# Kernel optimization log

Measured on AMD Instinct MI355X. Metric: run time of the kernel, lower is better.

## Reference

```python
import jax, jax.numpy as jnp
import numpy as np

D_MODEL = 1024
NHEAD = 16
HEAD_DIM = D_MODEL // NHEAD
NEG = -1e9
LN_EPS = 1e-5


def setup_inputs() -> dict:
    key = jax.random.key(0)
    ks = jax.random.split(key, 12)
    B, S, D = 2, 2048, D_MODEL
    scale = 1.0 / np.sqrt(D)
    inp = {
        "x": jax.random.normal(ks[0], (B, S, D), jnp.float32),
        "mask": jax.random.randint(ks[1], (B, S), 0, 2, jnp.int32),
        "wq": jax.random.normal(ks[2], (D, D), jnp.float32) * scale,
        "bq": jnp.zeros((D,), jnp.float32),
        "wk": jax.random.normal(ks[3], (D, D), jnp.float32) * scale,
        "bk": jnp.zeros((D,), jnp.float32),
        "wv": jax.random.normal(ks[4], (D, D), jnp.float32) * scale,
        "bv": jnp.zeros((D,), jnp.float32),
        "wo": jax.random.normal(ks[5], (D, D), jnp.float32) * scale,
        "bo": jnp.zeros((D,), jnp.float32),
        "attn_bias": jax.random.normal(ks[6], (1, NHEAD, 1, 1), jnp.float32) * 0.02,
        "ln_g": jnp.ones((D,), jnp.float32),
        "ln_b": jnp.zeros((D,), jnp.float32),
    }
    return inp


def _layer_norm(x, g, b):
    mu = jnp.mean(x, axis=-1, keepdims=True)
    var = jnp.var(x, axis=-1, keepdims=True)
    return (x - mu) * jax.lax.rsqrt(var + LN_EPS) * g + b


def reference(x, mask, wq, bq, wk, bk, wv, bv, wo, bo, attn_bias, ln_g, ln_b):
    B, S, D = x.shape
    H, Hd = NHEAD, HEAD_DIM
    # QKV projections -> [B, H, S, Hd]
    q = (x @ wq + bq).reshape(B, S, H, Hd).transpose(0, 2, 1, 3)
    k = (x @ wk + bk).reshape(B, S, H, Hd).transpose(0, 2, 1, 3)
    v = (x @ wv + bv).reshape(B, S, H, Hd).transpose(0, 2, 1, 3)
    # Scores [B, H, S, S] with per-head scalar bias
    scores = jnp.einsum("bhsd,bhtd->bhst", q, k) / jnp.sqrt(jnp.float32(Hd))
    scores = scores + attn_bias
    # mask [B,S] -> [B,1,1,S]; masked_fill where mask == 0
    m = (mask[:, None, None, :] == 0)
    scores = jnp.where(m, jnp.float32(NEG), scores)
    attn = jax.nn.softmax(scores, axis=-1)  # dropout = identity (eval)
    out = jnp.einsum("bhst,bhtd->bhsd", attn, v)
    out = out.transpose(0, 2, 1, 3).reshape(B, S, D)
    out = out @ wo + bo
    return _layer_norm(x + out, ln_g, ln_b)
```

## Files before the change

### kernel.cpp

```cpp
#include <hip/hip_runtime.h>

typedef __attribute__((ext_vector_type(8))) short short8;
typedef __attribute__((ext_vector_type(4))) float f32x4;
typedef __attribute__((ext_vector_type(16))) float f32x16;
typedef __attribute__((ext_vector_type(4))) unsigned short us4;

#define DEV __device__ __forceinline__

#define GLD16(gp, lp) __builtin_amdgcn_global_load_lds( \
    (const __attribute__((address_space(1))) void*)(gp), \
    (__attribute__((address_space(3))) void*)(lp), 16, 0, 0)

DEV unsigned short f2bf(float f) {
    union { float f; unsigned u; } v; v.f = f;
    unsigned r = v.u + 0x7fffu + ((v.u >> 16) & 1u);
    return (unsigned short)(r >> 16);
}

DEV float bf2f(unsigned short u) {
    union { unsigned u; float f; } v; v.u = (unsigned)u << 16;
    return v.f;
}

DEV float fexp2(float x) {
#if __has_builtin(__builtin_amdgcn_exp2f)
    return __builtin_amdgcn_exp2f(x);
#else
    return __expf(x * 0.69314718056f);
#endif
}

__global__ __launch_bounds__(256) void k_convert(const float* __restrict__ x,
                                                 unsigned short* __restrict__ xb) {
    int i = blockIdx.x * 256 + threadIdx.x;
    float4 v = ((const float4*)x)[i];
    us4 o = { f2bf(v.x), f2bf(v.y), f2bf(v.z), f2bf(v.w) };
    ((us4*)xb)[i] = o;
}

__global__ __launch_bounds__(256) void k_transw(const float* __restrict__ wq, const float* __restrict__ wk,
                                                const float* __restrict__ wv, const float* __restrict__ wo,
                                                unsigned short* __restrict__ wt) {
    __shared__ float tile[32][33];
    const int z = blockIdx.z;
    const float* src = (z == 0) ? wq : (z == 1) ? wk : (z == 2) ? wv : wo;
    unsigned short* dst = wt + (size_t)z * (1u << 20);
    const int n0 = blockIdx.x * 32, k0 = blockIdx.y * 32;
    const int tx = threadIdx.x, ty = threadIdx.y;
#pragma unroll
    for (int i = 0; i < 4; ++i)
        tile[ty + i * 8][tx] = src[(size_t)(k0 + ty + i * 8) * 1024 + n0 + tx];
    __syncthreads();
#pragma unroll
    for (int i = 0; i < 4; ++i)
        dst[(size_t)(n0 + ty + i * 8) * 1024 + k0 + tx] = f2bf(tile[tx][ty + i * 8]);
}

__global__ __launch_bounds__(256) void k_gemm_qkv(const unsigned short* __restrict__ A,
                                                  const unsigned short* __restrict__ Wt,
                                                  const float* __restrict__ bq,
                                                  const float* __restrict__ bk,
                                                  const float* __restrict__ bv,
                                                  unsigned short* __restrict__ Qo,
                                                  unsigned short* __restrict__ Ko,
                                                  unsigned short* __restrict__ Vo,
                                                  float qscale) {
    __shared__ unsigned short lA[2][128 * 32];
    __shared__ unsigned short lB[2][3][64 * 32];
    const int m0 = blockIdx.y * 128, n0 = blockIdx.x * 64;
    const int tid = threadIdx.x;
    const int lane = tid & 63;
    const int w = tid >> 6, wm = w >> 1, wn = w & 1;

    const int arow0 = tid >> 2, acl = tid & 3;
    const int arow1 = (tid + 256) >> 2;
    const int brow = tid >> 2;
    const unsigned short* agp0 = A + (size_t)(m0 + arow0) * 1024 + acl * 8;
    const unsigned short* agp1 = A + (size_t)(m0 + arow1) * 1024 + acl * 8;
    const unsigned short* bgp[3];
#pragma unroll
    for (int z = 0; z < 3; ++z)
        bgp[z] = Wt + ((size_t)z << 20) + (size_t)(n0 + brow) * 1024 + acl * 8;
    const int apc0 = ((arow0 << 2) | (acl ^ ((arow0 >> 1) & 3))) * 8;
    const int apc1 = ((arow1 << 2) | (acl ^ ((arow1 >> 1) & 3))) * 8;
    const int bpc  = ((brow  << 2) | (acl ^ ((brow  >> 1) & 3))) * 8;

    int ach[4], bch[2];
#pragma unroll
    for (int mt = 0; mt < 4; ++mt) {
        int row = wm * 64 + mt * 16 + (lane & 15);
        ach[mt] = ((row << 2) | ((lane >> 4) ^ ((row >> 1) & 3))) * 8;
    }
#pragma unroll
    for (int nt = 0; nt < 2; ++nt) {
        int row = wn * 32 + nt * 16 + (lane & 15);
        bch[nt] = ((row << 2) | ((lane >> 4) ^ ((row >> 1) & 3))) * 8;
    }

    f32x4 acc[3][4][2] = {};
    short8 ra0 = *(const short8*)agp0;
    short8 ra1 = *(const short8*)agp1;
    short8 rb[3];
#pragma unroll
    for (int z = 0; z < 3; ++z) rb[z] = *(const short8*)bgp[z];

    for (int t = 0; t < 32; ++t) {
        unsigned short* sA = lA[t & 1];
        *(short8*)(sA + apc0) = ra0;
        *(short8*)(sA + apc1) = ra1;
#pragma unroll
        for (int z = 0; z < 3; ++z)
            *(short8*)(lB[t & 1][z] + bpc) = rb[z];
        if (t < 31) {
            ra0 = *(const short8*)(agp0 + (t + 1) * 32);
            ra1 = *(const short8*)(agp1 + (t + 1) * 32);
#pragma unroll
            for (int z = 0; z < 3; ++z) rb[z] = *(const short8*)(bgp[z] + (t + 1) * 32);
        }
        __syncthreads();
        short8 af[4], bf[3][2];
#pragma unroll
        for (int mt = 0; mt < 4; ++mt) af[mt] = *(const short8*)(sA + ach[mt]);
#pragma unroll
        for (int z = 0; z < 3; ++z)
#pragma unroll
            for (int nt = 0; nt < 2; ++nt) bf[z][nt] = *(const short8*)(lB[t & 1][z] + bch[nt]);
#pragma unroll
        for (int z = 0; z < 3; ++z)
#pragma unroll
            for (int mt = 0; mt < 4; ++mt)
#pragma unroll
                for (int nt = 0; nt < 2; ++nt)
                    acc[z][mt][nt] = __builtin_amdgcn_mfma_f32_16x16x32_bf16(af[mt], bf[z][nt], acc[z][mt][nt], 0, 0, 0);
    }

#pragma unroll
    for (int z = 0; z < 3; ++z) {
        const float* bias = (z == 0) ? bq : (z == 1) ? bk : bv;
        const float scl = (z == 0) ? qscale : 1.0f;
        unsigned short* outp = (z == 0) ? Qo : (z == 1) ? Ko : Vo;
#pragma unroll
        for (int nt = 0; nt < 2; ++nt) {
            const int col = n0 + wn * 32 + nt * 16 + (lane & 15);
            const float bvv = bias[col];
            const int h = col >> 6, hd = col & 63;
#pragma unroll
            for (int mt = 0; mt < 4; ++mt) {
#pragma unroll
                for (int r = 0; r < 4; ++r) {
                    const int row = m0 + wm * 64 + mt * 16 + (lane >> 4) * 4 + r;
                    const int b = row >> 11, s = row & 2047;
                    const float v = (acc[z][mt][nt][r] + bvv) * scl;
                    if (z == 2)
                        outp[(size_t)((b * 16 + h) * 64 + hd) * 2048 + s] = f2bf(v);
                    else
                        outp[(size_t)((b * 16 + h) * 2048 + s) * 64 + hd] = f2bf(v);
                }
            }
        }
    }
}

__global__ __launch_bounds__(256) void k_gemm_o(const unsigned short* __restrict__ A,
                                                const unsigned short* __restrict__ Wt,
                                                const float* __restrict__ bias,
                                                unsigned short* __restrict__ out) {
    __shared__ unsigned short lA[2][128 * 32];
    __shared__ unsigned short lB[2][64 * 32];
    const int m0 = blockIdx.y * 128, n0 = blockIdx.x * 64;
    const int tid = threadIdx.x;
    const int lane = tid & 63;
    const int w = tid >> 6, wm = w >> 1, wn = w & 1;

    const int arow0 = tid >> 2, acl = tid & 3;
    const int arow1 = (tid + 256) >> 2;
    const int brow = tid >> 2;
    const unsigned short* agp0 = A + (size_t)(m0 + arow0) * 1024 + acl * 8;
    const unsigned short* agp1 = A + (size_t)(m0 + arow1) * 1024 + acl * 8;
    const unsigned short* bgp  = Wt + (size_t)(n0 + brow) * 1024 + acl * 8;
    const int apc0 = ((arow0 << 2) | (acl ^ ((arow0 >> 1) & 3))) * 8;
    const int apc1 = ((arow1 << 2) | (acl ^ ((arow1 >> 1) & 3))) * 8;
    const int bpc  = ((brow  << 2) | (acl ^ ((brow  >> 1) & 3))) * 8;

    int ach[4], bch[2];
#pragma unroll
    for (int mt = 0; mt < 4; ++mt) {
        int row = wm * 64 + mt * 16 + (lane & 15);
        ach[mt] = ((row << 2) | ((lane >> 4) ^ ((row >> 1) & 3))) * 8;
    }
#pragma unroll
    for (int nt = 0; nt < 2; ++nt) {
        int row = wn * 32 + nt * 16 + (lane & 15);
        bch[nt] = ((row << 2) | ((lane >> 4) ^ ((row >> 1) & 3))) * 8;
    }

    f32x4 acc[4][2] = {};
    short8 ra0 = *(const short8*)agp0;
    short8 ra1 = *(const short8*)agp1;
    short8 rb0 = *(const short8*)bgp;

    for (int t = 0; t < 32; ++t) {
        unsigned short* sA = lA[t & 1];
        unsigned short* sB = lB[t & 1];
        *(short8*)(sA + apc0) = ra0;
        *(short8*)(sA + apc1) = ra1;
        *(short8*)(sB + bpc)  = rb0;
        if (t < 31) {
            ra0 = *(const short8*)(agp0 + (t + 1) * 32);
            ra1 = *(const short8*)(agp1 + (t + 1) * 32);
            rb0 = *(const short8*)(bgp  + (t + 1) * 32);
        }
        __syncthreads();
        short8 af[4], bf[2];
#pragma unroll
        for (int mt = 0; mt < 4; ++mt) af[mt] = *(const short8*)(sA + ach[mt]);
#pragma unroll
        for (int nt = 0; nt < 2; ++nt) bf[nt] = *(const short8*)(sB + bch[nt]);
#pragma unroll
        for (int mt = 0; mt < 4; ++mt)
#pragma unroll
            for (int nt = 0; nt < 2; ++nt)
                acc[mt][nt] = __builtin_amdgcn_mfma_f32_16x16x32_bf16(af[mt], bf[nt], acc[mt][nt], 0, 0, 0);
    }

#pragma unroll
    for (int nt = 0; nt < 2; ++nt) {
        const int col = n0 + wn * 32 + nt * 16 + (lane & 15);
        const float bv = bias[col];
#pragma unroll
        for (int mt = 0; mt < 4; ++mt)
#pragma unroll
            for (int r = 0; r < 4; ++r) {
                const int row = m0 + wm * 64 + mt * 16 + (lane >> 4) * 4 + r;
                out[(size_t)row * 1024 + col] = f2bf(acc[mt][nt][r] + bv);
            }
    }
}

__global__ __launch_bounds__(256, 4) void k_attn(const unsigned short* __restrict__ Qb,
                                                 const unsigned short* __restrict__ Kb,
                                                 const unsigned short* __restrict__ Vt,
                                                 const int* __restrict__ mask,
                                                 const float* __restrict__ attn_bias,
                                                 unsigned short* __restrict__ po0,
                                                 unsigned short* __restrict__ po1,
                                                 float* __restrict__ lp0,
                                                 float* __restrict__ lp1) {
    __shared__ unsigned short ksm[2 * 4096];
    __shared__ unsigned short vsm[2 * 4096];
    __shared__ float addb[1024];
    const int id = blockIdx.x;
    const int xcd = id & 7, slot = id >> 3;
    const int half = slot & 1, qt = (slot >> 1) & 15, bh = xcd * 4 + (slot >> 5);
    const int b = bh >> 4, h = bh & 15;
    const int tid = threadIdx.x, l = tid & 63, w = tid >> 6;
    const int q = l & 31, hi = l >> 5;

    {
        const float hb = attn_bias[h] * 1.44269504f;
        int4 m = ((const int4*)(mask + b * 2048 + half * 1024))[tid];
        float4 a = { m.x ? hb : -1e30f, m.y ? hb : -1e30f,
                     m.z ? hb : -1e30f, m.w ? hb : -1e30f };
        ((float4*)addb)[tid] = a;
    }

    const size_t bhS = (size_t)bh * 2048;
    const unsigned short* Kbh = Kb + (bhS + half * 1024) * 64;
    const unsigned short* Vbh = Vt + (size_t)bh * 64 * 2048;
    const int q0 = qt * 128 + w * 32;

    const int srow = l >> 3;
    const int sxor = 8 * ((l & 7) ^ ((l >> 3) & 7));
    const unsigned short* Ksrc = Kbh + (size_t)(w * 16 + srow) * 64 + sxor;
    const unsigned short* Vsrc = Vbh + (size_t)(w * 16 + srow) * 2048 + half * 1024 + sxor;
    unsigned short* lk0 = ksm + w * 1024;
    unsigned short* lv0 = vsm + w * 1024;

#define STAGE(kt_, buf_) { \
    const unsigned short* gk = Ksrc + (size_t)(kt_) * 4096; \
    const unsigned short* gv = Vsrc + (kt_) * 64; \
    unsigned short* lk = lk0 + (buf_) * 4096; \
    unsigned short* lv = lv0 + (buf_) * 4096; \
    GLD16(gk, lk); GLD16(gk + 512, lk + 512); \
    GLD16(gv, lv); GLD16(gv + 16384, lv + 512); }

    int kro[2][4], vro[2][2][2];
#pragma unroll
    for (int sub = 0; sub < 2; ++sub) {
#pragma unroll
        for (int db = 0; db < 4; ++db) {
            int key = q + sub * 32;
            kro[sub][db] = key * 128 + ((db * 32 + hi * 16) ^ ((key & 7) << 4));
        }
#pragma unroll
        for (int kg = 0; kg < 2; ++kg)
#pragma unroll
            for (int dh = 0; dh < 2; ++dh) {
                int row = q + dh * 32;
                vro[sub][kg][dh] = row * 128 + ((sub * 64 + kg * 32 + hi * 16) ^ ((row & 7) << 4));
            }
    }

    short8 qf[4];
#pragma unroll
    for (int db = 0; db < 4; ++db)
        qf[db] = *(const short8*)(Qb + (bhS + q0 + q) * 64 + db * 16 + hi * 8);

    f32x16 o0 = {}, o1 = {};
    float4 ls = { 0.f, 0.f, 0.f, 0.f };

    STAGE(0, 0);
    __syncthreads();

    for (int kt = 0; kt < 16; ++kt) {
        const int cur = kt & 1;
        if (kt < 15) STAGE(kt + 1, cur ^ 1);
        const char* kb = (const char*)(ksm + cur * 4096);
        const char* vb = (const char*)(vsm + cur * 4096);
        const float* abp = addb + kt * 64;
#pragma unroll
        for (int sub = 0; sub < 2; ++sub) {
            short8 kf0 = *(const short8*)(kb + kro[sub][0]);
            short8 kf1 = *(const short8*)(kb + kro[sub][1]);
            short8 kf2 = *(const short8*)(kb + kro[sub][2]);
            short8 kf3 = *(const short8*)(kb + kro[sub][3]);
            f32x16 sa0 = {}, sa1 = {};
            __builtin_amdgcn_s_setprio(1);
            sa0 = __builtin_amdgcn_mfma_f32_32x32x16_bf16(kf0, qf[0], sa0, 0, 0, 0);
            sa1 = __builtin_amdgcn_mfma_f32_32x32x16_bf16(kf1, qf[1], sa1, 0, 0, 0);
            sa0 = __builtin_amdgcn_mfma_f32_32x32x16_bf16(kf2, qf[2], sa0, 0, 0, 0);
            sa1 = __builtin_amdgcn_mfma_f32_32x32x16_bf16(kf3, qf[3], sa1, 0, 0, 0);
            __builtin_amdgcn_s_setprio(0);
            float p[16];
#pragma unroll
            for (int rr = 0; rr < 4; ++rr) {
                float4 ab = *(const float4*)(abp + sub * 32 + rr * 8 + hi * 4);
                p[rr * 4 + 0] = fexp2(sa0[rr * 4 + 0] + sa1[rr * 4 + 0] + ab.x);
                p[rr * 4 + 1] = fexp2(sa0[rr * 4 + 1] + sa1[rr * 4 + 1] + ab.y);
                p[rr * 4 + 2] = fexp2(sa0[rr * 4 + 2] + sa1[rr * 4 + 2] + ab.z);
                p[rr * 4 + 3] = fexp2(sa0[rr * 4 + 3] + sa1[rr * 4 + 3] + ab.w);
            }
#pragma unroll
            for (int r = 0; r < 16; r += 4) {
                ls.x += p[r]; ls.y += p[r + 1]; ls.z += p[r + 2]; ls.w += p[r + 3];
            }
#pragma unroll
            for (int kg = 0; kg < 2; ++kg) {
                unsigned P0, P1, P2, P3;
                asm("v_cvt_pk_bf16_f32 %0, %1, %2" : "=v"(P0) : "v"(p[kg * 8 + 0]), "v"(p[kg * 8 + 1]));
                asm("v_cvt_pk_bf16_f32 %0, %1, %2" : "=v"(P1) : "v"(p[kg * 8 + 2]), "v"(p[kg * 8 + 3]));
                asm("v_cvt_pk_bf16_f32 %0, %1, %2" : "=v"(P2) : "v"(p[kg * 8 + 4]), "v"(p[kg * 8 + 5]));
                asm("v_cvt_pk_bf16_f32 %0, %1, %2" : "=v"(P3) : "v"(p[kg * 8 + 6]), "v"(p[kg * 8 + 7]));
                asm("v_permlane32_swap_b32 %0, %1" : "+v"(P0), "+v"(P2));
                asm("v_permlane32_swap_b32 %0, %1" : "+v"(P1), "+v"(P3));
                union { unsigned u[4]; short8 s8; } af;
                af.u[0] = P0; af.u[1] = P1; af.u[2] = P2; af.u[3] = P3;
                short8 vf0 = *(const short8*)(vb + vro[sub][kg][0]);
                short8 vf1 = *(const short8*)(vb + vro[sub][kg][1]);
                __builtin_amdgcn_s_setprio(1);
                o0 = __builtin_amdgcn_mfma_f32_32x32x16_bf16(af.s8, vf0, o0, 0, 0, 0);
                o1 = __builtin_amdgcn_mfma_f32_32x32x16_bf16(af.s8, vf1, o1, 0, 0, 0);
                __builtin_amdgcn_s_setprio(0);
            }
        }
        __syncthreads();
    }
#undef STAGE

    float lsum = ls.x + ls.y + ls.z + ls.w;
    lsum += __shfl_xor(lsum, 32, 64);
    float* lpx = half ? lp1 : lp0;
    if (hi == 0) lpx[bhS + q0 + q] = lsum;
    unsigned short* pop = (half ? po1 : po0) + ((size_t)b * 2048 + q0) * 1024 + h * 64 + q;
#pragma unroll
    for (int r = 0; r < 16; ++r) {
        int qrow = (r & 3) + 8 * (r >> 2) + 4 * hi;
        pop[(size_t)qrow * 1024] = f2bf(o0[r]);
        pop[(size_t)qrow * 1024 + 32] = f2bf(o1[r]);
    }
}

__global__ __launch_bounds__(256) void k_comb(const unsigned short* __restrict__ po0,
                                              const unsigned short* __restrict__ po1,
                                              const float* __restrict__ lp0,
                                              const float* __restrict__ lp1,
                                              unsigned short* __restrict__ ao) {
    const int idx8 = blockIdx.x * 256 + threadIdx.x;
    const int e = idx8 * 8;
    const int row = e >> 10, c = e & 1023;
    const int h = c >> 6, b = row >> 11, s = row & 2047;
    const size_t li = ((size_t)(b * 16 + h) << 11) + s;
    const float rinv = __builtin_amdgcn_rcpf(lp0[li] + lp1[li]);
    short8 a0 = ((const short8*)po0)[idx8];
    short8 a1 = ((const short8*)po1)[idx8];
    short8 o;
#pragma unroll
    for (int j = 0; j < 8; ++j)
        o[j] = (short)f2bf((bf2f((unsigned short)a0[j]) + bf2f((unsigned short)a1[j])) * rinv);
    ((short8*)ao)[idx8] = o;
}

__global__ __launch_bounds__(256) void k_ln(const float* __restrict__ x, const unsigned short* __restrict__ op,
                                            const float* __restrict__ g, const float* __restrict__ be,
                                            float* __restrict__ out) {
    const int row = blockIdx.x, tid = threadIdx.x;
    const float4 xv = ((const float4*)(x + (size_t)row * 1024))[tid];
    const us4 ov = ((const us4*)(op + (size_t)row * 1024))[tid];
    float4 v = { xv.x + bf2f(ov.x), xv.y + bf2f(ov.y), xv.z + bf2f(ov.z), xv.w + bf2f(ov.w) };
    float sum = v.x + v.y + v.z + v.w;
    float ss = v.x * v.x + v.y * v.y + v.z * v.z + v.w * v.w;
#pragma unroll
    for (int xm = 1; xm < 64; xm <<= 1) {
        sum += __shfl_xor(sum, xm, 64);
        ss += __shfl_xor(ss, xm, 64);
    }
    __shared__ float red[8];
    const int lane = tid & 63, w = tid >> 6;
    if (lane == 0) { red[w] = sum; red[4 + w] = ss; }
    __syncthreads();
    sum = red[0] + red[1] + red[2] + red[3];
    ss = red[4] + red[5] + red[6] + red[7];
    const float mu = sum * (1.0f / 1024.0f);
    const float rstd = rsqrtf(ss * (1.0f / 1024.0f) - mu * mu + 1e-5f);
    const float4 gv = ((const float4*)g)[tid];
    const float4 bv = ((const float4*)be)[tid];
    float4 o = { (v.x - mu) * rstd * gv.x + bv.x, (v.y - mu) * rstd * gv.y + bv.y,
                 (v.z - mu) * rstd * gv.z + bv.z, (v.w - mu) * rstd * gv.w + bv.w };
    ((float4*)(out + (size_t)row * 1024))[tid] = o;
}

extern "C" void kernel_launch(void* const* d_in, const int* in_sizes, int n_in,
                              void* d_out, int out_size, void* d_ws, size_t ws_size,
                              hipStream_t stream) {
    const float* x        = (const float*)d_in[0];
    const int*   mask     = (const int*)d_in[1];
    const float* wq       = (const float*)d_in[2];
    const float* bq       = (const float*)d_in[3];
    const float* wk       = (const float*)d_in[4];
    const float* bk       = (const float*)d_in[5];
    const float* wv       = (const float*)d_in[6];
    const float* bv       = (const float*)d_in[7];
    const float* wo       = (const float*)d_in[8];
    const float* bo       = (const float*)d_in[9];
    const float* attnb    = (const float*)d_in[10];
    const float* ln_g     = (const float*)d_in[11];
    const float* ln_b     = (const float*)d_in[12];

    char* ws = (char*)d_ws;
    unsigned short* xb  = (unsigned short*)(ws);
    unsigned short* wt  = (unsigned short*)(ws + (8ll  << 20));
    unsigned short* qb  = (unsigned short*)(ws + (16ll << 20));
    unsigned short* kb  = (unsigned short*)(ws + (24ll << 20));
    unsigned short* vtb = (unsigned short*)(ws + (32ll << 20));
    unsigned short* po1 = (unsigned short*)(ws + (40ll << 20));
    float*          lp0 = (float*)(ws + (48ll << 20));
    float*          lp1 = (float*)(ws + (48ll << 20) + (256ll << 10));
    unsigned short* po0 = xb;
    unsigned short* ao  = qb;
    unsigned short* opj = kb;

    const float qscale = 0.125f * 1.44269504f;

    k_convert<<<4096, 256, 0, stream>>>(x, xb);
    k_transw<<<dim3(32, 32, 4), dim3(32, 8), 0, stream>>>(wq, wk, wv, wo, wt);
    k_gemm_qkv<<<dim3(16, 32), 256, 0, stream>>>(xb, wt, bq, bk, bv, qb, kb, vtb, qscale);
    k_attn<<<1024, 256, 0, stream>>>(qb, kb, vtb, mask, attnb, po0, po1, lp0, lp1);
    k_comb<<<2048, 256, 0, stream>>>(po0, po1, lp0, lp1, ao);
    k_gemm_o<<<dim3(16, 32), 256, 0, stream>>>(ao, wt + (3u << 20), bo, opj);
    k_ln<<<4096, 256, 0, stream>>>(x, opj, ln_g, ln_b, (float*)d_out);
}
```

Baseline: 132.8 us.

## Compute softmax row sums via MFMA with ones and fold bias into accumulator init

Replaces the per-lane VALU accumulation of softmax denominators and the cross-lane shuffle with an extra MFMA that multiplies the bf16 probabilities by a ones matrix, producing row sums in an accumulator. It also seeds the QK score accumulator with the additive bias/mask values and chains all four MFMAs into one accumulator, removing the separate add before exp2. This trades VALU work for one more MFMA per PV step plus a serial MFMA dependency chain. Row sums are now computed from bf16-rounded probabilities, which matches the numerator rounding.

```diff
diff --git a/kernel.cpp b/kernel.cpp
--- a/kernel.cpp
+++ b/kernel.cpp
@@ -306,8 +306,11 @@
     for (int db = 0; db < 4; ++db)
         qf[db] = *(const short8*)(Qb + (bhS + q0 + q) * 64 + db * 16 + hi * 8);
 
-    f32x16 o0 = {}, o1 = {};
-    float4 ls = { 0.f, 0.f, 0.f, 0.f };
+    short8 ones;
+#pragma unroll
+    for (int j = 0; j < 8; ++j) ones[j] = (short)0x3F80;
+
+    f32x16 o0 = {}, o1 = {}, ol = {};
 
     STAGE(0, 0);
     __syncthreads();
@@ -324,26 +327,20 @@
             short8 kf1 = *(const short8*)(kb + kro[sub][1]);
             short8 kf2 = *(const short8*)(kb + kro[sub][2]);
             short8 kf3 = *(const short8*)(kb + kro[sub][3]);
-            f32x16 sa0 = {}, sa1 = {};
+            union { f32x16 v; float4 f4[4]; } sa;
+#pragma unroll
+            for (int rr = 0; rr < 4; ++rr)
+                sa.f4[rr] = *(const float4*)(abp + sub * 32 + rr * 8 + hi * 4);
             __builtin_amdgcn_s_setprio(1);
-            sa0 = __builtin_amdgcn_mfma_f32_32x32x16_bf16(kf0, qf[0], sa0, 0, 0, 0);
-            sa1 = __builtin_amdgcn_mfma_f32_32x32x16_bf16(kf1, qf[1], sa1, 0, 0, 0);
-            sa0 = __builtin_amdgcn_mfma_f32_32x32x16_bf16(kf2, qf[2], sa0, 0, 0, 0);
-            sa1 = __builtin_amdgcn_mfma_f32_32x32x16_bf16(kf3, qf[3], sa1, 0, 0, 0);
+            sa.v = __builtin_amdgcn_mfma_f32_32x32x16_bf16(kf0, qf[0], sa.v, 0, 0, 0);
+            sa.v = __builtin_amdgcn_mfma_f32_32x32x16_bf16(kf1, qf[1], sa.v, 0, 0, 0);
+            sa.v = __builtin_amdgcn_mfma_f32_32x32x16_bf16(kf2, qf[2], sa.v, 0, 0, 0);
+            sa.v = __builtin_amdgcn_mfma_f32_32x32x16_bf16(kf3, qf[3], sa.v, 0, 0, 0);
             __builtin_amdgcn_s_setprio(0);
             float p[16];
 #pragma unroll
-            for (int rr = 0; rr < 4; ++rr) {
-                float4 ab = *(const float4*)(abp + sub * 32 + rr * 8 + hi * 4);
-                p[rr * 4 + 0] = fexp2(sa0[rr * 4 + 0] + sa1[rr * 4 + 0] + ab.x);
-                p[rr * 4 + 1] = fexp2(sa0[rr * 4 + 1] + sa1[rr * 4 + 1] + ab.y);
-                p[rr * 4 + 2] = fexp2(sa0[rr * 4 + 2] + sa1[rr * 4 + 2] + ab.z);
-                p[rr * 4 + 3] = fexp2(sa0[rr * 4 + 3] + sa1[rr * 4 + 3] + ab.w);
-            }
-#pragma unroll
-            for (int r = 0; r < 16; r += 4) {
-                ls.x += p[r]; ls.y += p[r + 1]; ls.z += p[r + 2]; ls.w += p[r + 3];
-            }
+            for (int r = 0; r < 16; ++r)
+                p[r] = fexp2(sa.v[r]);
 #pragma unroll
             for (int kg = 0; kg < 2; ++kg) {
                 unsigned P0, P1, P2, P3;
@@ -360,6 +357,7 @@
                 __builtin_amdgcn_s_setprio(1);
                 o0 = __builtin_amdgcn_mfma_f32_32x32x16_bf16(af.s8, vf0, o0, 0, 0, 0);
                 o1 = __builtin_amdgcn_mfma_f32_32x32x16_bf16(af.s8, vf1, o1, 0, 0, 0);
+                ol = __builtin_amdgcn_mfma_f32_32x32x16_bf16(af.s8, ones, ol, 0, 0, 0);
                 __builtin_amdgcn_s_setprio(0);
             }
         }
@@ -367,10 +365,12 @@
     }
 #undef STAGE
 
-    float lsum = ls.x + ls.y + ls.z + ls.w;
-    lsum += __shfl_xor(lsum, 32, 64);
     float* lpx = half ? lp1 : lp0;
-    if (hi == 0) lpx[bhS + q0 + q] = lsum;
+    if (q == 0) {
+#pragma unroll
+        for (int r = 0; r < 16; ++r)
+            lpx[bhS + q0 + (r & 3) + 8 * (r >> 2) + 4 * hi] = ol[r];
+    }
     unsigned short* pop = (half ? po1 : po0) + ((size_t)b * 2048 + q0) * 1024 + h * 64 + q;
 #pragma unroll
     for (int r = 0; r < 16; ++r) {
```

New measurement: 130.4 us. No clear change (-1.9%).
